# Performance work log

Hardware: AMD Instinct MI355X
Metric: run time of the kernel (lower is better)

## Reference

```python
import jax, jax.numpy as jnp
import numpy as np
from jax.scipy.special import logsumexp

NEG = -1e9  # stands in for log(0) = -inf in the padded one-hots (avoids NaN-producing -inf)


def setup_inputs() -> dict:
    key = jax.random.key(0)
    ks = jax.random.split(key, 9)
    Lx, Ly, B, D, Vout = 64, 64, 128, 256, 53
    return {
        "prior_ctx": jax.random.normal(ks[0], (Lx, B, D), dtype=jnp.float32),
        "modern_ctx": jax.random.normal(ks[1], (Ly, B, D), dtype=jnp.float32),
        "W_sub": jax.random.normal(ks[2], (Vout, D), dtype=jnp.float32) * 0.05,
        "b_sub": jax.random.normal(ks[3], (Vout,), dtype=jnp.float32) * 0.05,
        "W_ins": jax.random.normal(ks[4], (Vout, D), dtype=jnp.float32) * 0.05,
        "b_ins": jax.random.normal(ks[5], (Vout,), dtype=jnp.float32) * 0.05,
        "target_ids": jax.random.randint(ks[6], (Ly - 1, B), 0, Vout, dtype=jnp.int32),
        "src_lengths": jax.random.randint(ks[7], (B,), 1, Lx + 1),
        "tgt_lengths": jax.random.randint(ks[8], (B,), 1, Ly + 1),
    }


def reference(prior_ctx, modern_ctx, W_sub, b_sub, W_ins, b_ins,
              target_ids, src_lengths, tgt_lengths):
    Lx, B, D = prior_ctx.shape
    Ly = modern_ctx.shape[0]
    Vout = W_sub.shape[0]

    # outer-sum context: [Lx, Ly, B, D]
    ctx = prior_ctx[:, None, :, :] + modern_ctx[None, :, :, :]

    # padding matrix: True where both source pos i and target pos j are valid. [Lx, Ly, B, 1]
    mask = ((jnp.arange(Lx)[:, None, None] < src_lengths[None, None, :])
            & (jnp.arange(Ly)[None, :, None] < tgt_lengths[None, None, :]))[..., None]

    # heads: Linear + LogSoftmax, zeroed on padding. [Lx, Ly, B, Vout]
    sub = jnp.where(mask, jax.nn.log_softmax(jnp.einsum('xybd,vd->xybv', ctx, W_sub) + b_sub, axis=-1), 0.0)
    ins = jnp.where(mask, jax.nn.log_softmax(jnp.einsum('xybd,vd->xybv', ctx, W_ins) + b_ins, axis=-1), 0.0)

    del_probs = sub[:, :, :, Vout - 1]  # [Lx, Ly, B]
    end_probs = ins[:, :, :, Vout - 1]

    # log one-hots of targets shifted by 1: [Ly-1, B, Vout]
    log_oh = jnp.where(target_ids[:, :, None] == jnp.arange(Vout)[None, None, :], 0.0, NEG)

    sub_probs = logsumexp(sub[:, :-1] + log_oh[None], axis=-1)  # [Lx, Ly-1, B]
    ins_probs = logsumexp(ins[:, :-1] + log_oh[None], axis=-1)
    return del_probs, end_probs, sub_probs, ins_probs
```

## Files before the change

### kernel.cpp

```cpp
#include <hip/hip_runtime.h>

#define D   256
#define NB  128
#define NV  53
#define NR  8192
#define V4  14
#define SLB (V4*NR*4)
#define ESOFF (4*SLB)
#define WBOFF (8*SLB)
#define BTOFF (WBOFF + 3584*8)
#define A52   (13*NR*4)
#define LOG2E 1.44269504088896340736f
#define LN2   0.69314718055994530942f


typedef float  f4 __attribute__((ext_vector_type(4)));
typedef float  f2 __attribute__((ext_vector_type(2)));
typedef short  s8 __attribute__((ext_vector_type(8)));

__device__ __forceinline__ ushort f2bf(float f) {
    uint u = __float_as_uint(f);
    u += 0x7fff + ((u >> 16) & 1);
    return (ushort)(u >> 16);
}
__device__ __forceinline__ float bflo(uint w) { return __uint_as_float(w << 16); }
__device__ __forceinline__ float bfhi(uint w) { return __uint_as_float(w & 0xffff0000u); }
__device__ __forceinline__ float fexp2(float x) { return __builtin_exp2f(x); }
__device__ __forceinline__ float flog2(float x) { return __builtin_log2f(x); }

__global__ void p0_kernel(const float* __restrict__ Wsub, const float* __restrict__ Wins,
                          const float* __restrict__ bsub, const float* __restrict__ bins,
                          ushort* __restrict__ WBg, float* __restrict__ biasT)
{
    const int F  = blockIdx.x * 64 + threadIdx.x;
    const int l  = F & 63, s = (F >> 6) & 7, nt = F >> 9;
    const int o  = nt * 16 + (l & 15);
    const int d0 = 32 * s + 8 * (l >> 4);
    s8 bfr;
    if (o < NV) {
        const float* w = Wsub + o * D + d0;
        #pragma unroll
        for (int j = 0; j < 8; ++j) bfr[j] = (short)f2bf(w[j] * LOG2E);
    } else if (o < 106) {
        const float* w = Wins + (o - NV) * D + d0;
        #pragma unroll
        for (int j = 0; j < 8; ++j) bfr[j] = (short)f2bf(w[j] * LOG2E);
    } else {
        #pragma unroll
        for (int j = 0; j < 8; ++j) bfr[j] = 0;
    }
    *(s8*)&WBg[F * 8] = bfr;
    if (F < 112) {
        float bv = 0.f;
        if (F < NV)       bv = bsub[F] * LOG2E;
        else if (F < 106) bv = bins[F - NV] * LOG2E;
        biasT[F] = bv;
    }
}

template<int NT0, int NTN>
__device__ __forceinline__ void p1_body(
    const float* __restrict__ prior, const float* __restrict__ modern,
    const ushort* __restrict__ WBg, const float* __restrict__ biasT,
    ushort* __restrict__ wsb, ushort* __restrict__ WB, int tid, int tg)
{
    #pragma unroll
    for (int i = 0; i < NTN * 2; ++i) {
        const int idx = i * 256 + tid;
        *(s8*)&WB[idx * 8] = *(const s8*)&WBg[(NT0 * 512 + idx) * 8];
    }
    __syncthreads();

    const int wave = tid >> 6, lane = tid & 63;
    const int tile = tg * 4 + wave;
    const int side = tile >> 9;
    const int row0 = (tile & 511) << 4;
    const int lrow = lane & 15, lk = lane >> 4;
    const float* __restrict__ src =
        (side ? modern : prior) + (size_t)(row0 + lrow) * D + lk * 8;

    f4 acc[NTN];
    #pragma unroll
    for (int j = 0; j < NTN; ++j) { acc[j][0]=0.f; acc[j][1]=0.f; acc[j][2]=0.f; acc[j][3]=0.f; }

    #pragma unroll
    for (int s = 0; s < 8; ++s) {
        const f4 c0 = *(const f4*)(src + 32 * s);
        const f4 c1 = *(const f4*)(src + 32 * s + 4);
        s8 a;
        a[0]=(short)f2bf(c0[0]); a[1]=(short)f2bf(c0[1]);
        a[2]=(short)f2bf(c0[2]); a[3]=(short)f2bf(c0[3]);
        a[4]=(short)f2bf(c1[0]); a[5]=(short)f2bf(c1[1]);
        a[6]=(short)f2bf(c1[2]); a[7]=(short)f2bf(c1[3]);
        #pragma unroll
        for (int j = 0; j < NTN; ++j) {
            const s8 bfr = *(const s8*)&WB[(((j << 3) + s) * 64 + lane) * 8];
            acc[j] = __builtin_amdgcn_mfma_f32_16x16x32_bf16(a, bfr, acc[j], 0, 0, 0);
        }
    }

    #pragma unroll
    for (int j = 0; j < NTN; ++j) {
        const int v = (NT0 + j) * 16 + lrow;
        const float bias = side ? biasT[v] : 0.f;
        const bool valid = v < 106;
        const bool isS   = v < NV;
        const int  vi    = isS ? v : v - NV;
        ushort* __restrict__ raw = wsb + (size_t)(side * 2 + (isS ? 0 : 1)) * SLB;
        ushort* __restrict__ Eb  = raw + ESOFF;
        const int a0 = (vi >> 2) * (NR * 4) + (vi & 3);
        #pragma unroll
        for (int r = 0; r < 4; ++r) {
            if (valid) {
                const int row = row0 + 4 * lk + r;
                const float val = acc[j][r] + bias;
                raw[a0 + row * 4] = f2bf(val);
                Eb[a0 + row * 4]  = f2bf(fexp2(val));
            }
        }
    }
    if (NT0 == 4) {
        if (lrow >= 10 && lrow <= 12) {
            const int vi = 43 + lrow;
            const int a0 = (vi >> 2) * (NR * 4) + (vi & 3);
            #pragma unroll
            for (int r = 0; r < 4; ++r) {
                const int row = row0 + 4 * lk + r;
                wsb[ESOFF + (size_t)(side * 2 + 0) * SLB + a0 + row * 4] = 0;
                wsb[ESOFF + (size_t)(side * 2 + 1) * SLB + a0 + row * 4] = 0;
            }
        }
    }
}

__global__ __launch_bounds__(256) void p1_kernel(
    const float* __restrict__ prior, const float* __restrict__ modern,
    const ushort* __restrict__ WBg, const float* __restrict__ biasT,
    ushort* __restrict__ wsb)
{
    __shared__ ushort WB[4 * 512 * 8];
    const int tid = threadIdx.x;
    const int tg  = blockIdx.x >> 1;
    if ((blockIdx.x & 1) == 0)
        p1_body<0, 4>(prior, modern, WBg, biasT, wsb, WB, tid, tg);
    else
        p1_body<4, 3>(prior, modern, WBg, biasT, wsb, WB, tid, tg);
}

__global__ __launch_bounds__(256) void p2_kernel(
    const ushort* __restrict__ wsb,
    const int* __restrict__ target, const int* __restrict__ srclen,
    const int* __restrict__ tgtlen, float* __restrict__ out)
{
    const int tid = threadIdx.x;
    const int b   = tid & 127;
    const int bid = blockIdx.x;
    const int xt  = ((bid & 7) << 1) | ((bid >> 3) & 1);
    const int y   = ((bid >> 4) << 1) | (tid >> 7);
    const int yb  = y * NB + b;

    const int sl = srclen[b], tl = tgtlen[b];
    const bool ymask = y < tl;
    const bool hasT  = y < 63;
    const int  t     = hasT ? target[y * NB + b] : 0;
    const int  toff  = (t >> 2) * (NR * 4) + (t & 3);

    #pragma unroll 1
    for (int dist = 0; dist < 2; ++dist) {
        const ushort* __restrict__ Praw = wsb + dist * SLB;
        const ushort* __restrict__ Mraw = wsb + (2 + dist) * SLB;
        const ushort* __restrict__ PE   = Praw + ESOFF;
        const ushort* __restrict__ ME   = Mraw + ESOFF;

        f2 em0[V4], em1[V4];
        #pragma unroll
        for (int g = 0; g < V4; ++g) {
            const uint2 q = *(const uint2*)(ME + (g * NR + yb) * 4);
            em0[g][0] = bflo(q.x); em0[g][1] = bfhi(q.x);
            em1[g][0] = bflo(q.y); em1[g][1] = bfhi(q.y);
        }
        const float mlt = bflo((uint)Mraw[toff + yb * 4]);
        const float m52 = bflo((uint)Mraw[A52  + yb * 4]);

        float* __restrict__ o0 = out + dist * 524288;
        float* __restrict__ o1 = out + 1048576 + dist * 516096;

        #pragma unroll
        for (int xi = 0; xi < 4; ++xi) {
            const int x  = (xt << 2) + xi;
            const int xb = x * NB + b;
            const bool msk = (x < sl) & ymask;

            f2 s0; s0[0] = 0.f; s0[1] = 0.f;
            f2 s1; s1[0] = 0.f; s1[1] = 0.f;
            #pragma unroll
            for (int g = 0; g < V4; ++g) {
                const uint2 p = *(const uint2*)(PE + (g * NR + xb) * 4);
                f2 a; a[0] = bflo(p.x); a[1] = bfhi(p.x);
                f2 c; c[0] = bflo(p.y); c[1] = bfhi(p.y);
                s0 += a * em0[g];
                s1 += c * em1[g];
            }
            const float S  = (s0[0] + s0[1]) + (s1[0] + s1[1]);
            const float ls = flog2(S);

            const float l52 = bflo((uint)Praw[A52 + xb * 4]) + m52;
            o0[((x << 6) | y) * NB + b] = msk ? (l52 - ls) * LN2 : 0.f;
            if (hasT) {
                const float lt = bflo((uint)Praw[toff + xb * 4]) + mlt;
                o1[(x * 63 + y) * NB + b] = msk ? (lt - ls) * LN2 : 0.f;
            }
        }
    }
}

extern "C" void kernel_launch(void* const* d_in, const int* in_sizes, int n_in,
                              void* d_out, int out_size, void* d_ws, size_t ws_size,
                              hipStream_t stream) {
    const float* prior  = (const float*)d_in[0];
    const float* modern = (const float*)d_in[1];
    const float* Wsub   = (const float*)d_in[2];
    const float* bsub   = (const float*)d_in[3];
    const float* Wins   = (const float*)d_in[4];
    const float* bins   = (const float*)d_in[5];
    const int*   target = (const int*)d_in[6];
    const int*   srclen = (const int*)d_in[7];
    const int*   tgtlen = (const int*)d_in[8];
    ushort* wsb   = (ushort*)d_ws;
    ushort* WBg   = wsb + WBOFF;
    float*  biasT = (float*)(wsb + BTOFF);
    float*  out   = (float*)d_out;

    p0_kernel<<<56, 64, 0, stream>>>(Wsub, Wins, bsub, bins, WBg, biasT);
    p1_kernel<<<512, 256, 0, stream>>>(prior, modern, WBg, biasT, wsb);
    p2_kernel<<<512, 256, 0, stream>>>(wsb, target, srclen, tgtlen, out);
}
```

Baseline: 38.07 us.

## Repack vocab layout, drop LDS weight staging, split p1 into single-wave blocks

The ins head is realigned to start at vocab index 56 so each 4-vocab group is contiguous and padded to a 16-wide tile. That lets p1 use swapped MFMA operands and write 4 bf16 values per store instead of scattered 16-bit stores. p1 now reads weights straight from global/L2 without LDS staging or a barrier, and runs as 4096 single-wave blocks. p2 doubles its block count with half the x-range per block for more parallelism, at the cost of reloading the modern-side exp values more often.

```diff
diff --git a/kernel.cpp b/kernel.cpp
--- a/kernel.cpp
+++ b/kernel.cpp
@@ -4,12 +4,11 @@
 #define NB  128
 #define NV  53
 #define NR  8192
-#define V4  14
-#define SLB (V4*NR*4)
-#define ESOFF (4*SLB)
-#define WBOFF (8*SLB)
+#define NG  28
+#define SLB (NG*NR*4)
+#define ESOFF (2*SLB)
+#define WBOFF (4*SLB)
 #define BTOFF (WBOFF + 3584*8)
-#define A52   (13*NR*4)
 #define LOG2E 1.44269504088896340736f
 #define LN2   0.69314718055994530942f
 
@@ -34,15 +33,13 @@
 {
     const int F  = blockIdx.x * 64 + threadIdx.x;
     const int l  = F & 63, s = (F >> 6) & 7, nt = F >> 9;
-    const int o  = nt * 16 + (l & 15);
+    const int u  = nt * 16 + (l & 15);
     const int d0 = 32 * s + 8 * (l >> 4);
+    const float* w = nullptr;
+    if (u < NV)                  w = Wsub + u * D + d0;
+    else if (u >= 56 && u <= 108) w = Wins + (u - 56) * D + d0;
     s8 bfr;
-    if (o < NV) {
-        const float* w = Wsub + o * D + d0;
-        #pragma unroll
-        for (int j = 0; j < 8; ++j) bfr[j] = (short)f2bf(w[j] * LOG2E);
-    } else if (o < 106) {
-        const float* w = Wins + (o - NV) * D + d0;
+    if (w) {
         #pragma unroll
         for (int j = 0; j < 8; ++j) bfr[j] = (short)f2bf(w[j] * LOG2E);
     } else {
@@ -52,36 +49,27 @@
     *(s8*)&WBg[F * 8] = bfr;
     if (F < 112) {
         float bv = 0.f;
-        if (F < NV)       bv = bsub[F] * LOG2E;
-        else if (F < 106) bv = bins[F - NV] * LOG2E;
+        if (F < NV)                  bv = bsub[F] * LOG2E;
+        else if (F >= 56 && F <= 108) bv = bins[F - 56] * LOG2E;
         biasT[F] = bv;
     }
 }
 
-template<int NT0, int NTN>
+template<int NT0, int NNT>
 __device__ __forceinline__ void p1_body(
     const float* __restrict__ prior, const float* __restrict__ modern,
     const ushort* __restrict__ WBg, const float* __restrict__ biasT,
-    ushort* __restrict__ wsb, ushort* __restrict__ WB, int tid, int tg)
-{
-    #pragma unroll
-    for (int i = 0; i < NTN * 2; ++i) {
-        const int idx = i * 256 + tid;
-        *(s8*)&WB[idx * 8] = *(const s8*)&WBg[(NT0 * 512 + idx) * 8];
-    }
-    __syncthreads();
-
-    const int wave = tid >> 6, lane = tid & 63;
-    const int tile = tg * 4 + wave;
+    ushort* __restrict__ wsb, int lane, int tile)
+{
     const int side = tile >> 9;
     const int row0 = (tile & 511) << 4;
     const int lrow = lane & 15, lk = lane >> 4;
     const float* __restrict__ src =
         (side ? modern : prior) + (size_t)(row0 + lrow) * D + lk * 8;
 
-    f4 acc[NTN];
+    f4 acc[NNT];
     #pragma unroll
-    for (int j = 0; j < NTN; ++j) { acc[j][0]=0.f; acc[j][1]=0.f; acc[j][2]=0.f; acc[j][3]=0.f; }
+    for (int j = 0; j < NNT; ++j) { acc[j][0]=0.f; acc[j][1]=0.f; acc[j][2]=0.f; acc[j][3]=0.f; }
 
     #pragma unroll
     for (int s = 0; s < 8; ++s) {
@@ -93,58 +81,48 @@
         a[4]=(short)f2bf(c1[0]); a[5]=(short)f2bf(c1[1]);
         a[6]=(short)f2bf(c1[2]); a[7]=(short)f2bf(c1[3]);
         #pragma unroll
-        for (int j = 0; j < NTN; ++j) {
-            const s8 bfr = *(const s8*)&WB[(((j << 3) + s) * 64 + lane) * 8];
-            acc[j] = __builtin_amdgcn_mfma_f32_16x16x32_bf16(a, bfr, acc[j], 0, 0, 0);
-        }
-    }
-
+        for (int j = 0; j < NNT; ++j) {
+            const s8 wf = *(const s8*)&WBg[((((NT0 + j) << 3) + s) * 64 + lane) * 8];
+            acc[j] = __builtin_amdgcn_mfma_f32_16x16x32_bf16(wf, a, acc[j], 0, 0, 0);
+        }
+    }
+
+    ushort* __restrict__ raw = wsb + (size_t)side * SLB;
+    ushort* __restrict__ Eb  = raw + ESOFF;
+    const int row = row0 + lrow;
     #pragma unroll
-    for (int j = 0; j < NTN; ++j) {
-        const int v = (NT0 + j) * 16 + lrow;
-        const float bias = side ? biasT[v] : 0.f;
-        const bool valid = v < 106;
-        const bool isS   = v < NV;
-        const int  vi    = isS ? v : v - NV;
-        ushort* __restrict__ raw = wsb + (size_t)(side * 2 + (isS ? 0 : 1)) * SLB;
-        ushort* __restrict__ Eb  = raw + ESOFF;
-        const int a0 = (vi >> 2) * (NR * 4) + (vi & 3);
+    for (int j = 0; j < NNT; ++j) {
+        const int u0 = (NT0 + j) * 16 + 4 * lk;
+        f4 bias;
+        if (side) bias = *(const f4*)&biasT[u0];
+        else      { bias[0]=0.f; bias[1]=0.f; bias[2]=0.f; bias[3]=0.f; }
+        ushort rq[4], eq[4];
         #pragma unroll
         for (int r = 0; r < 4; ++r) {
-            if (valid) {
-                const int row = row0 + 4 * lk + r;
-                const float val = acc[j][r] + bias;
-                raw[a0 + row * 4] = f2bf(val);
-                Eb[a0 + row * 4]  = f2bf(fexp2(val));
-            }
-        }
-    }
-    if (NT0 == 4) {
-        if (lrow >= 10 && lrow <= 12) {
-            const int vi = 43 + lrow;
-            const int a0 = (vi >> 2) * (NR * 4) + (vi & 3);
-            #pragma unroll
-            for (int r = 0; r < 4; ++r) {
-                const int row = row0 + 4 * lk + r;
-                wsb[ESOFF + (size_t)(side * 2 + 0) * SLB + a0 + row * 4] = 0;
-                wsb[ESOFF + (size_t)(side * 2 + 1) * SLB + a0 + row * 4] = 0;
-            }
-        }
-    }
-}
-
-__global__ __launch_bounds__(256) void p1_kernel(
+            const int u = u0 + r;
+            const float val = acc[j][r] + bias[r];
+            rq[r] = f2bf(val);
+            const bool pad = (u > 52 && u < 56) || (u > 108);
+            eq[r] = pad ? (ushort)0 : f2bf(fexp2(val));
+        }
+        const int addr = (u0 >> 2) * (NR * 4) + row * 4;
+        *(uint2*)&raw[addr] = *(uint2*)rq;
+        *(uint2*)&Eb[addr]  = *(uint2*)eq;
+    }
+}
+
+__global__ __launch_bounds__(64) void p1_kernel(
     const float* __restrict__ prior, const float* __restrict__ modern,
     const ushort* __restrict__ WBg, const float* __restrict__ biasT,
     ushort* __restrict__ wsb)
 {
-    __shared__ ushort WB[4 * 512 * 8];
-    const int tid = threadIdx.x;
-    const int tg  = blockIdx.x >> 1;
-    if ((blockIdx.x & 1) == 0)
-        p1_body<0, 4>(prior, modern, WBg, biasT, wsb, WB, tid, tg);
-    else
-        p1_body<4, 3>(prior, modern, WBg, biasT, wsb, WB, tid, tg);
+    const int lane  = threadIdx.x;
+    const int chunk = blockIdx.x & 3;
+    const int tile  = blockIdx.x >> 2;
+    if (chunk == 0)      p1_body<0, 2>(prior, modern, WBg, biasT, wsb, lane, tile);
+    else if (chunk == 1) p1_body<2, 2>(prior, modern, WBg, biasT, wsb, lane, tile);
+    else if (chunk == 2) p1_body<4, 2>(prior, modern, WBg, biasT, wsb, lane, tile);
+    else                 p1_body<6, 1>(prior, modern, WBg, biasT, wsb, lane, tile);
 }
 
 __global__ __launch_bounds__(256) void p2_kernel(
@@ -155,47 +133,50 @@
     const int tid = threadIdx.x;
     const int b   = tid & 127;
     const int bid = blockIdx.x;
-    const int xt  = ((bid & 7) << 1) | ((bid >> 3) & 1);
-    const int y   = ((bid >> 4) << 1) | (tid >> 7);
+    const int xt  = ((bid & 7) << 2) | ((bid >> 3) & 3);
+    const int y   = ((bid >> 5) << 1) | (tid >> 7);
     const int yb  = y * NB + b;
 
     const int sl = srclen[b], tl = tgtlen[b];
     const bool ymask = y < tl;
     const bool hasT  = y < 63;
     const int  t     = hasT ? target[y * NB + b] : 0;
-    const int  toff  = (t >> 2) * (NR * 4) + (t & 3);
+
+    const ushort* __restrict__ Praw = wsb;
+    const ushort* __restrict__ Mraw = wsb + SLB;
+    const ushort* __restrict__ PE   = wsb + 2 * SLB;
+    const ushort* __restrict__ ME   = wsb + 3 * SLB;
 
     #pragma unroll 1
     for (int dist = 0; dist < 2; ++dist) {
-        const ushort* __restrict__ Praw = wsb + dist * SLB;
-        const ushort* __restrict__ Mraw = wsb + (2 + dist) * SLB;
-        const ushort* __restrict__ PE   = Praw + ESOFF;
-        const ushort* __restrict__ ME   = Mraw + ESOFF;
-
-        f2 em0[V4], em1[V4];
-        #pragma unroll
-        for (int g = 0; g < V4; ++g) {
-            const uint2 q = *(const uint2*)(ME + (g * NR + yb) * 4);
+        const int g0   = dist * 14;
+        const int tbase = (g0 + (t >> 2)) * (NR * 4) + (t & 3);
+        const int a52b  = (g0 + 13) * (NR * 4);
+
+        f2 em0[14], em1[14];
+        #pragma unroll
+        for (int g = 0; g < 14; ++g) {
+            const uint2 q = *(const uint2*)(ME + ((g0 + g) * NR + yb) * 4);
             em0[g][0] = bflo(q.x); em0[g][1] = bfhi(q.x);
             em1[g][0] = bflo(q.y); em1[g][1] = bfhi(q.y);
         }
-        const float mlt = bflo((uint)Mraw[toff + yb * 4]);
-        const float m52 = bflo((uint)Mraw[A52  + yb * 4]);
+        const float mlt = bflo((uint)Mraw[tbase + yb * 4]);
+        const float m52 = bflo((uint)Mraw[a52b  + yb * 4]);
 
         float* __restrict__ o0 = out + dist * 524288;
         float* __restrict__ o1 = out + 1048576 + dist * 516096;
 
         #pragma unroll
-        for (int xi = 0; xi < 4; ++xi) {
-            const int x  = (xt << 2) + xi;
+        for (int xi = 0; xi < 2; ++xi) {
+            const int x  = xt * 2 + xi;
             const int xb = x * NB + b;
             const bool msk = (x < sl) & ymask;
 
             f2 s0; s0[0] = 0.f; s0[1] = 0.f;
             f2 s1; s1[0] = 0.f; s1[1] = 0.f;
             #pragma unroll
-            for (int g = 0; g < V4; ++g) {
-                const uint2 p = *(const uint2*)(PE + (g * NR + xb) * 4);
+            for (int g = 0; g < 14; ++g) {
+                const uint2 p = *(const uint2*)(PE + ((g0 + g) * NR + xb) * 4);
                 f2 a; a[0] = bflo(p.x); a[1] = bfhi(p.x);
                 f2 c; c[0] = bflo(p.y); c[1] = bfhi(p.y);
                 s0 += a * em0[g];
@@ -204,10 +185,10 @@
             const float S  = (s0[0] + s0[1]) + (s1[0] + s1[1]);
             const float ls = flog2(S);
 
-            const float l52 = bflo((uint)Praw[A52 + xb * 4]) + m52;
+            const float l52 = bflo((uint)Praw[a52b + xb * 4]) + m52;
             o0[((x << 6) | y) * NB + b] = msk ? (l52 - ls) * LN2 : 0.f;
             if (hasT) {
-                const float lt = bflo((uint)Praw[toff + xb * 4]) + mlt;
+                const float lt = bflo((uint)Praw[tbase + xb * 4]) + mlt;
                 o1[(x * 63 + y) * NB + b] = msk ? (lt - ls) * LN2 : 0.f;
             }
         }
@@ -232,6 +213,6 @@
     float*  out   = (float*)d_out;
 
     p0_kernel<<<56, 64, 0, stream>>>(Wsub, Wins, bsub, bins, WBg, biasT);
-    p1_kernel<<<512, 256, 0, stream>>>(prior, modern, WBg, biasT, wsb);
-    p2_kernel<<<512, 256, 0, stream>>>(wsb, target, srclen, tgtlen, out);
-}
+    p1_kernel<<<4096, 64, 0, stream>>>(prior, modern, WBg, biasT, wsb);
+    p2_kernel<<<1024, 256, 0, stream>>>(wsb, target, srclen, tgtlen, out);
+}
```

New measurement: 42.57 us. 1.12x slower.
